# Performance work log

Hardware: AMD Instinct MI355X
Metric: run time of the kernel (lower is better)

Reference implementation:

```python
import jax, jax.numpy as jnp
import numpy as np

DIM = 768
EPS = 1e-06


def _layernorm(x, gamma, beta):
    # LayerNorm over last axis (channels), eps=EPS, elementwise affine
    mu = jnp.mean(x, axis=-1, keepdims=True)
    var = jnp.mean(jnp.square(x - mu), axis=-1, keepdims=True)
    return (x - mu) * jax.lax.rsqrt(var + EPS) * gamma + beta


def setup_inputs() -> dict:
    key = jax.random.key(0)
    ks = jax.random.split(key, 10)
    B, C, H, W = 16, DIM, 32, 32
    s = 1.0 / np.sqrt(C)  # mimic Conv2d default init scale
    return {
        "x": jax.random.normal(ks[0], (B, C, H, W), dtype=jnp.float32),
        "W1": jax.random.uniform(ks[1], (C, C), jnp.float32, -s, s),
        "b1": jax.random.uniform(ks[2], (C,), jnp.float32, -s, s),
        "g1": jnp.ones((C,), jnp.float32),
        "beta1": jnp.zeros((C,), jnp.float32),
        "W2": jax.random.uniform(ks[3], (C, C), jnp.float32, -s, s),
        "b2": jax.random.uniform(ks[4], (C,), jnp.float32, -s, s),
        "g2": jnp.ones((C,), jnp.float32),
        "beta2": jnp.zeros((C,), jnp.float32),
        "W3": jax.random.uniform(ks[5], (C, C), jnp.float32, -s, s),
        "b3": jax.random.uniform(ks[6], (C,), jnp.float32, -s, s),
    }


def reference(x, W1, b1, g1, beta1, W2, b2, g2, beta2, W3, b3):
    # x: [B, C, H, W] (NCHW). Work in NHWC; 1x1 conv == channel matmul.
    h = jnp.transpose(x, (0, 2, 3, 1))  # [B, H, W, C]
    h = jnp.einsum("bhwc,oc->bhwo", h, W1) + b1
    h = jax.nn.gelu(_layernorm(h, g1, beta1), approximate=False)
    h = jnp.einsum("bhwc,oc->bhwo", h, W2) + b2
    h = jax.nn.gelu(_layernorm(h, g2, beta2), approximate=False)
    h = jnp.einsum("bhwc,oc->bhwo", h, W3) + b3
    return jnp.transpose(h, (0, 3, 1, 2))  # back to NCHW
```

## Files before the change

### kernel.cpp

```cpp
#include <hip/hip_runtime.h>
#include <hip/hip_bf16.h>

typedef __bf16 bf16;
typedef __bf16 bf16x4 __attribute__((ext_vector_type(4)));
typedef __bf16 bf16x8 __attribute__((ext_vector_type(8)));
typedef float f32x4 __attribute__((ext_vector_type(4)));

#define DIM 768
#define HW 1024
#define BATCH 16
#define M_TOTAL (BATCH * HW)
#define NKT 24

#define AS1 __attribute__((address_space(1)))
#define AS3 __attribute__((address_space(3)))


__global__ void wcvt3_kernel(const float4* __restrict__ w1, const float4* __restrict__ w2,
                             const float4* __restrict__ w3,
                             bf16x8* __restrict__ o1, bf16x8* __restrict__ o2,
                             bf16x8* __restrict__ o3) {
    const int b = blockIdx.x;
    const int which = b / 288;
    const int i = (b % 288) * 256 + threadIdx.x;
    const float4* w = which == 0 ? w1 : which == 1 ? w2 : w3;
    bf16x8* o = which == 0 ? o1 : which == 1 ? o2 : o3;
    const int row = i / 96, br = i % 96;
    const int q = br >> 2, g = br & 3;
    float4 lo = w[row * 192 + q * 8 + g];
    float4 hi = w[row * 192 + q * 8 + g + 4];
    bf16x8 r = { (bf16)lo.x, (bf16)lo.y, (bf16)lo.z, (bf16)lo.w,
                 (bf16)hi.x, (bf16)hi.y, (bf16)hi.z, (bf16)hi.w };
    o[row * 96 + br] = r;
}

__global__ void transpose_cvt_kernel(const float* __restrict__ x, bf16* __restrict__ xb) {
    __shared__ float tile[32][33];
    const int b = blockIdx.z;
    const int hw0 = blockIdx.x * 32;
    const int c0 = blockIdx.y * 32;
    const int tx = threadIdx.x, ty = threadIdx.y;

    const float* src = x + ((size_t)b * DIM + c0) * HW + hw0;
#pragma unroll
    for (int j = 0; j < 4; j++)
        tile[ty + 8 * j][tx] = src[(size_t)(ty + 8 * j) * HW + tx];
    __syncthreads();
    const int ptx = (((tx & 15) >> 2) << 3) + (tx & 3) + ((tx >> 4) << 2);
    bf16* dst = xb + ((size_t)b * HW + hw0) * DIM + c0;
#pragma unroll
    for (int j = 0; j < 4; j++)
        dst[(size_t)(ty + 8 * j) * DIM + ptx] = (bf16)tile[tx][ty + 8 * j];
}

template <int MODE>
__global__ __launch_bounds__(256, 3) void gemm_kernel(
    const bf16* __restrict__ A,
    const bf16* __restrict__ Bw,
    const float* __restrict__ bias,
    void* __restrict__ out)
{
    constexpr int K = DIM;
    __shared__ bf16 As[3][128][32];
    __shared__ bf16 Bs[3][128][32];

    const int t = threadIdx.x;
    const int lane = t & 63;
    const int wave = t >> 6;
    const int wr = wave >> 1, wc = wave & 1;

    const int bid = blockIdx.x;
    const int virt = (bid & 7) * 96 + (bid >> 3);
    const int mI = virt / 6;
    const int m0 = mI * 128;
    const int n0 = (virt - mI * 6) * 128;

    const int fr = lane & 15;
    const int fq = lane >> 4;

    f32x4 acc[4][4] = {};

    const int sr = t >> 2;
    const int sb = t & 3;

    auto stage = [&](int kt, int buf) {
        const int k0 = kt * 32;
#pragma unroll
        for (int j = 0; j < 2; j++) {
            const int r = sr + j * 64;
            const int gs = sb ^ ((r ^ (r >> 2)) & 3);
            __builtin_amdgcn_global_load_lds(
                (const AS1 void*)(A + (size_t)(m0 + r) * K + k0 + gs * 8),
                (AS3 void*)&As[buf][r][sb * 8], 16, 0, 0);
            __builtin_amdgcn_global_load_lds(
                (const AS1 void*)(Bw + (size_t)(n0 + r) * K + k0 + gs * 8),
                (AS3 void*)&Bs[buf][r][sb * 8], 16, 0, 0);
        }
    };

    stage(0, 0);
    stage(1, 1);
    asm volatile("s_waitcnt vmcnt(4)" ::: "memory");
    __builtin_amdgcn_s_barrier();
    __builtin_amdgcn_sched_barrier(0);

    int c0 = 0, c1 = 1, c2 = 2;
    for (int kt = 0; kt < NKT; ++kt) {
        if (kt + 2 < NKT) stage(kt + 2, c2);

        bf16x8 aF[4], bF[4];
#pragma unroll
        for (int mi = 0; mi < 4; mi++) {
            const int R = wr * 64 + mi * 16 + fr;
            aF[mi] = *(const bf16x8*)(&As[c0][R][0] + ((fq ^ ((R ^ (R >> 2)) & 3)) << 3));
        }
#pragma unroll
        for (int ni = 0; ni < 4; ni++) {
            const int R = wc * 64 + ni * 16 + fr;
            bF[ni] = *(const bf16x8*)(&Bs[c0][R][0] + ((fq ^ ((R ^ (R >> 2)) & 3)) << 3));
        }
        __builtin_amdgcn_s_setprio(1);
#pragma unroll
        for (int mi = 0; mi < 4; mi++)
#pragma unroll
            for (int ni = 0; ni < 4; ni++)
                acc[mi][ni] = __builtin_amdgcn_mfma_f32_16x16x32_bf16(aF[mi], bF[ni], acc[mi][ni], 0, 0, 0);
        __builtin_amdgcn_s_setprio(0);

        if (kt < NKT - 1) {
            if (kt + 2 < NKT) { asm volatile("s_waitcnt vmcnt(4)" ::: "memory"); }
            else              { asm volatile("s_waitcnt vmcnt(0)" ::: "memory"); }
            __builtin_amdgcn_s_barrier();
            __builtin_amdgcn_sched_barrier(0);
        }
        const int tmp = c0; c0 = c1; c1 = c2; c2 = tmp;
    }

    if (MODE == 0) {
        bf16* o = (bf16*)out;
#pragma unroll
        for (int mi = 0; mi < 4; mi++) {
            const int row = m0 + wr * 64 + mi * 16 + fq * 4;
#pragma unroll
            for (int ni = 0; ni < 4; ni++) {
                const int col = n0 + wc * 64 + ni * 16 + fr;
                const int pcol = n0 + wc * 64 + ((ni >> 1) << 5) + ((fr >> 2) << 3)
                               + (fr & 3) + ((ni & 1) << 2);
                const float bv = bias[col];
#pragma unroll
                for (int r = 0; r < 4; r++)
                    o[(size_t)(row + r) * DIM + pcol] = (bf16)(acc[mi][ni][r] + bv);
            }
        }
    } else {
        float* o = (float*)out;
#pragma unroll
        for (int mi = 0; mi < 4; mi++) {
            const int nb = m0 + wr * 64 + mi * 16 + (lane >> 4) * 4;
            const int bI = nb >> 10, hw = nb & 1023;
#pragma unroll
            for (int ni = 0; ni < 4; ni++) {
                const int col = n0 + wc * 64 + ni * 16 + fr;
                f32x4 v = acc[mi][ni] + bias[col];
                *(f32x4*)(o + ((size_t)bI * DIM + col) * HW + hw) = v;
            }
        }
    }
}

__global__ __launch_bounds__(256) void ln_gelu_kernel(
    bf16* __restrict__ h, const float* __restrict__ g, const float* __restrict__ beta)
{
    const int wave = threadIdx.x >> 6;
    const int lane = threadIdx.x & 63;
    const int n = blockIdx.x * 4 + wave;
    bf16* row = h + (size_t)n * DIM;

    float v[12];
    float s = 0.f, ss = 0.f;
#pragma unroll
    for (int j = 0; j < 3; j++) {
        bf16x4 x = *(const bf16x4*)(row + j * 256 + lane * 4);
#pragma unroll
        for (int i = 0; i < 4; i++) {
            float f = (float)x[i];
            v[j * 4 + i] = f;
            s += f;
            ss += f * f;
        }
    }
#pragma unroll
    for (int off = 32; off > 0; off >>= 1) {
        s += __shfl_xor(s, off);
        ss += __shfl_xor(ss, off);
    }
    const float mu = s * (1.f / DIM);
    const float var = ss * (1.f / DIM) - mu * mu;
    const float rstd = rsqrtf(var + 1e-6f);

#pragma unroll
    for (int j = 0; j < 3; j++) {
        bf16x4 r;
#pragma unroll
        for (int i = 0; i < 4; i++) {
            const int c = j * 256 + lane * 4 + i;
            const int p = (lane * 4 + i) & 31;
            const int kk = ((p >> 3) << 2) + (p & 7) + ((p & 4) ? 12 : 0);
            const int gi = (c & ~31) + kk;
            float y = (v[j * 4 + i] - mu) * rstd * g[gi] + beta[gi];
            y = 0.5f * y * (1.f + erff(y * 0.70710678118f));
            r[i] = (bf16)y;
        }
        *(bf16x4*)(row + j * 256 + lane * 4) = r;
    }
}

extern "C" void kernel_launch(void* const* d_in, const int* in_sizes, int n_in,
                              void* d_out, int out_size, void* d_ws, size_t ws_size,
                              hipStream_t stream) {
    const float* x   = (const float*)d_in[0];
    const float* W1  = (const float*)d_in[1];
    const float* b1  = (const float*)d_in[2];
    const float* g1  = (const float*)d_in[3];
    const float* be1 = (const float*)d_in[4];
    const float* W2  = (const float*)d_in[5];
    const float* b2  = (const float*)d_in[6];
    const float* g2  = (const float*)d_in[7];
    const float* be2 = (const float*)d_in[8];
    const float* W3  = (const float*)d_in[9];
    const float* b3  = (const float*)d_in[10];
    float* out = (float*)d_out;

    bf16* Wb1  = (bf16*)d_ws;
    bf16* Wb2  = Wb1 + (size_t)DIM * DIM;
    bf16* Wb3  = Wb2 + (size_t)DIM * DIM;
    bf16* buf0 = Wb3 + (size_t)DIM * DIM;
    bf16* buf1 = buf0 + (size_t)M_TOTAL * DIM;

    wcvt3_kernel<<<864, 256, 0, stream>>>((const float4*)W1, (const float4*)W2, (const float4*)W3,
                                          (bf16x8*)Wb1, (bf16x8*)Wb2, (bf16x8*)Wb3);

    transpose_cvt_kernel<<<dim3(32, 24, 16), dim3(32, 8), 0, stream>>>(x, buf0);

    const int ggrid = (M_TOTAL / 128) * (DIM / 128);
    gemm_kernel<0><<<ggrid, 256, 0, stream>>>(buf0, Wb1, b1, buf1);
    ln_gelu_kernel<<<M_TOTAL / 4, 256, 0, stream>>>(buf1, g1, be1);
    gemm_kernel<0><<<ggrid, 256, 0, stream>>>(buf1, Wb2, b2, buf0);
    ln_gelu_kernel<<<M_TOTAL / 4, 256, 0, stream>>>(buf0, g2, be2);
    gemm_kernel<1><<<ggrid, 256, 0, stream>>>(buf0, Wb3, b3, out);
}
```

Baseline: 163.7 us.

## Retile GEMM to 64x192 double-buffered tiles and merge prep kernels

The GEMM tile changes from 128x128 with a triple-buffered pipeline to 64x192 with double buffering in one shared LDS array. Each of the four waves now covers all 64 rows and a 48-column slice, the grid grows to 1024 blocks, and launch bounds rise to allow four blocks per CU. The weight conversion and input transpose kernels are merged into one launch to save a kernel dispatch. The smaller tile lowers arithmetic intensity per LDS load, and the shallower pipeline waits vmcnt(0) every iteration, trading prefetch depth for occupancy.

```diff
diff --git a/kernel.cpp b/kernel.cpp
--- a/kernel.cpp
+++ b/kernel.cpp
@@ -16,136 +16,132 @@
 #define AS3 __attribute__((address_space(3)))
 
 
-__global__ void wcvt3_kernel(const float4* __restrict__ w1, const float4* __restrict__ w2,
-                             const float4* __restrict__ w3,
-                             bf16x8* __restrict__ o1, bf16x8* __restrict__ o2,
-                             bf16x8* __restrict__ o3) {
-    const int b = blockIdx.x;
-    const int which = b / 288;
-    const int i = (b % 288) * 256 + threadIdx.x;
-    const float4* w = which == 0 ? w1 : which == 1 ? w2 : w3;
-    bf16x8* o = which == 0 ? o1 : which == 1 ? o2 : o3;
-    const int row = i / 96, br = i % 96;
-    const int q = br >> 2, g = br & 3;
-    float4 lo = w[row * 192 + q * 8 + g];
-    float4 hi = w[row * 192 + q * 8 + g + 4];
-    bf16x8 r = { (bf16)lo.x, (bf16)lo.y, (bf16)lo.z, (bf16)lo.w,
-                 (bf16)hi.x, (bf16)hi.y, (bf16)hi.z, (bf16)hi.w };
-    o[row * 96 + br] = r;
-}
-
-__global__ void transpose_cvt_kernel(const float* __restrict__ x, bf16* __restrict__ xb) {
+__global__ void prep_kernel(const float* __restrict__ x, bf16* __restrict__ xb,
+                            const float4* __restrict__ w1, const float4* __restrict__ w2,
+                            const float4* __restrict__ w3,
+                            bf16x8* __restrict__ o1, bf16x8* __restrict__ o2,
+                            bf16x8* __restrict__ o3) {
     __shared__ float tile[32][33];
-    const int b = blockIdx.z;
-    const int hw0 = blockIdx.x * 32;
-    const int c0 = blockIdx.y * 32;
-    const int tx = threadIdx.x, ty = threadIdx.y;
-
-    const float* src = x + ((size_t)b * DIM + c0) * HW + hw0;
-#pragma unroll
-    for (int j = 0; j < 4; j++)
-        tile[ty + 8 * j][tx] = src[(size_t)(ty + 8 * j) * HW + tx];
-    __syncthreads();
-    const int ptx = (((tx & 15) >> 2) << 3) + (tx & 3) + ((tx >> 4) << 2);
-    bf16* dst = xb + ((size_t)b * HW + hw0) * DIM + c0;
-#pragma unroll
-    for (int j = 0; j < 4; j++)
-        dst[(size_t)(ty + 8 * j) * DIM + ptx] = (bf16)tile[tx][ty + 8 * j];
+    if (blockIdx.x < 864) {
+        const int b = blockIdx.x;
+        const int which = b / 288;
+        const int i = (b % 288) * 256 + threadIdx.x;
+        const float4* w = which == 0 ? w1 : which == 1 ? w2 : w3;
+        bf16x8* o = which == 0 ? o1 : which == 1 ? o2 : o3;
+        const int row = i / 96, br = i % 96;
+        const int q = br >> 2, g = br & 3;
+        float4 lo = w[row * 192 + q * 8 + g];
+        float4 hi = w[row * 192 + q * 8 + g + 4];
+        bf16x8 r = { (bf16)lo.x, (bf16)lo.y, (bf16)lo.z, (bf16)lo.w,
+                     (bf16)hi.x, (bf16)hi.y, (bf16)hi.z, (bf16)hi.w };
+        o[row * 96 + br] = r;
+    } else {
+        const int e = blockIdx.x - 864;
+        const int b = e / 768;
+        const int rem = e % 768;
+        const int c0 = (rem / 32) * 32;
+        const int hw0 = (rem % 32) * 32;
+        const int tx = threadIdx.x & 31, ty = threadIdx.x >> 5;
+
+        const float* src = x + ((size_t)b * DIM + c0) * HW + hw0;
+#pragma unroll
+        for (int j = 0; j < 4; j++)
+            tile[ty + 8 * j][tx] = src[(size_t)(ty + 8 * j) * HW + tx];
+        __syncthreads();
+        const int ptx = (((tx & 15) >> 2) << 3) + (tx & 3) + ((tx >> 4) << 2);
+        bf16* dst = xb + ((size_t)b * HW + hw0) * DIM + c0;
+#pragma unroll
+        for (int j = 0; j < 4; j++)
+            dst[(size_t)(ty + 8 * j) * DIM + ptx] = (bf16)tile[tx][ty + 8 * j];
+    }
 }
 
 template <int MODE>
-__global__ __launch_bounds__(256, 3) void gemm_kernel(
+__global__ __launch_bounds__(256, 4) void gemm_kernel(
     const bf16* __restrict__ A,
     const bf16* __restrict__ Bw,
     const float* __restrict__ bias,
     void* __restrict__ out)
 {
     constexpr int K = DIM;
-    __shared__ bf16 As[3][128][32];
-    __shared__ bf16 Bs[3][128][32];
+    __shared__ bf16 S[2][256][32];
 
     const int t = threadIdx.x;
     const int lane = t & 63;
-    const int wave = t >> 6;
-    const int wr = wave >> 1, wc = wave & 1;
+    const int w = t >> 6;
 
     const int bid = blockIdx.x;
-    const int virt = (bid & 7) * 96 + (bid >> 3);
-    const int mI = virt / 6;
-    const int m0 = mI * 128;
-    const int n0 = (virt - mI * 6) * 128;
-
-    const int fr = lane & 15;
-    const int fq = lane >> 4;
-
-    f32x4 acc[4][4] = {};
-
-    const int sr = t >> 2;
-    const int sb = t & 3;
+    const int virt = (bid & 7) * 128 + (bid >> 3);
+    const int m0 = (virt >> 2) * 64;
+    const int n0 = (virt & 3) * 192;
+
+    const int fr = lane & 15, fq = lane >> 4;
+
+    f32x4 acc[4][3] = {};
+
+    const int sg = t & 3;
 
     auto stage = [&](int kt, int buf) {
         const int k0 = kt * 32;
 #pragma unroll
-        for (int j = 0; j < 2; j++) {
-            const int r = sr + j * 64;
-            const int gs = sb ^ ((r ^ (r >> 2)) & 3);
-            __builtin_amdgcn_global_load_lds(
-                (const AS1 void*)(A + (size_t)(m0 + r) * K + k0 + gs * 8),
-                (AS3 void*)&As[buf][r][sb * 8], 16, 0, 0);
-            __builtin_amdgcn_global_load_lds(
-                (const AS1 void*)(Bw + (size_t)(n0 + r) * K + k0 + gs * 8),
-                (AS3 void*)&Bs[buf][r][sb * 8], 16, 0, 0);
+        for (int j = 0; j < 4; j++) {
+            const int r = j * 64 + (t >> 2);
+            const int gs = sg ^ ((r ^ (r >> 2)) & 3);
+            const bf16* src = (j == 0)
+                ? (A  + (size_t)(m0 + r) * K + k0 + gs * 8)
+                : (Bw + (size_t)(n0 + r - 64) * K + k0 + gs * 8);
+            __builtin_amdgcn_global_load_lds((const AS1 void*)src,
+                (AS3 void*)&S[buf][r][sg * 8], 16, 0, 0);
         }
     };
 
     stage(0, 0);
-    stage(1, 1);
-    asm volatile("s_waitcnt vmcnt(4)" ::: "memory");
+    asm volatile("s_waitcnt vmcnt(0)" ::: "memory");
     __builtin_amdgcn_s_barrier();
     __builtin_amdgcn_sched_barrier(0);
 
-    int c0 = 0, c1 = 1, c2 = 2;
+    int cur = 0;
     for (int kt = 0; kt < NKT; ++kt) {
-        if (kt + 2 < NKT) stage(kt + 2, c2);
-
-        bf16x8 aF[4], bF[4];
+        bf16x8 aF[4], bF[3];
 #pragma unroll
         for (int mi = 0; mi < 4; mi++) {
-            const int R = wr * 64 + mi * 16 + fr;
-            aF[mi] = *(const bf16x8*)(&As[c0][R][0] + ((fq ^ ((R ^ (R >> 2)) & 3)) << 3));
-        }
-#pragma unroll
-        for (int ni = 0; ni < 4; ni++) {
-            const int R = wc * 64 + ni * 16 + fr;
-            bF[ni] = *(const bf16x8*)(&Bs[c0][R][0] + ((fq ^ ((R ^ (R >> 2)) & 3)) << 3));
-        }
+            const int R = mi * 16 + fr;
+            aF[mi] = *(const bf16x8*)(&S[cur][R][0] + ((fq ^ ((R ^ (R >> 2)) & 3)) << 3));
+        }
+#pragma unroll
+        for (int ni = 0; ni < 3; ni++) {
+            const int R = 64 + w * 48 + ni * 16 + fr;
+            bF[ni] = *(const bf16x8*)(&S[cur][R][0] + ((fq ^ ((R ^ (R >> 2)) & 3)) << 3));
+        }
+        if (kt + 1 < NKT) stage(kt + 1, cur ^ 1);
+
         __builtin_amdgcn_s_setprio(1);
 #pragma unroll
         for (int mi = 0; mi < 4; mi++)
 #pragma unroll
-            for (int ni = 0; ni < 4; ni++)
+            for (int ni = 0; ni < 3; ni++)
                 acc[mi][ni] = __builtin_amdgcn_mfma_f32_16x16x32_bf16(aF[mi], bF[ni], acc[mi][ni], 0, 0, 0);
         __builtin_amdgcn_s_setprio(0);
 
-        if (kt < NKT - 1) {
-            if (kt + 2 < NKT) { asm volatile("s_waitcnt vmcnt(4)" ::: "memory"); }
-            else              { asm volatile("s_waitcnt vmcnt(0)" ::: "memory"); }
+        if (kt + 1 < NKT) {
+            asm volatile("s_waitcnt vmcnt(0)" ::: "memory");
             __builtin_amdgcn_s_barrier();
             __builtin_amdgcn_sched_barrier(0);
         }
-        const int tmp = c0; c0 = c1; c1 = c2; c2 = tmp;
+        cur ^= 1;
     }
 
     if (MODE == 0) {
         bf16* o = (bf16*)out;
 #pragma unroll
         for (int mi = 0; mi < 4; mi++) {
-            const int row = m0 + wr * 64 + mi * 16 + fq * 4;
-#pragma unroll
-            for (int ni = 0; ni < 4; ni++) {
-                const int col = n0 + wc * 64 + ni * 16 + fr;
-                const int pcol = n0 + wc * 64 + ((ni >> 1) << 5) + ((fr >> 2) << 3)
-                               + (fr & 3) + ((ni & 1) << 2);
+            const int row = m0 + mi * 16 + fq * 4;
+#pragma unroll
+            for (int ni = 0; ni < 3; ni++) {
+                const int off = w * 48 + ni * 16;
+                const int col = n0 + off + fr;
+                const int pcol = n0 + (off & ~31) + ((fr >> 2) << 3) + (fr & 3)
+                               + (((off >> 4) & 1) << 2);
                 const float bv = bias[col];
 #pragma unroll
                 for (int r = 0; r < 4; r++)
@@ -156,11 +152,11 @@
         float* o = (float*)out;
 #pragma unroll
         for (int mi = 0; mi < 4; mi++) {
-            const int nb = m0 + wr * 64 + mi * 16 + (lane >> 4) * 4;
+            const int nb = m0 + mi * 16 + fq * 4;
             const int bI = nb >> 10, hw = nb & 1023;
 #pragma unroll
-            for (int ni = 0; ni < 4; ni++) {
-                const int col = n0 + wc * 64 + ni * 16 + fr;
+            for (int ni = 0; ni < 3; ni++) {
+                const int col = n0 + w * 48 + ni * 16 + fr;
                 f32x4 v = acc[mi][ni] + bias[col];
                 *(f32x4*)(o + ((size_t)bI * DIM + col) * HW + hw) = v;
             }
@@ -237,12 +233,11 @@
     bf16* buf0 = Wb3 + (size_t)DIM * DIM;
     bf16* buf1 = buf0 + (size_t)M_TOTAL * DIM;
 
-    wcvt3_kernel<<<864, 256, 0, stream>>>((const float4*)W1, (const float4*)W2, (const float4*)W3,
-                                          (bf16x8*)Wb1, (bf16x8*)Wb2, (bf16x8*)Wb3);
-
-    transpose_cvt_kernel<<<dim3(32, 24, 16), dim3(32, 8), 0, stream>>>(x, buf0);
-
-    const int ggrid = (M_TOTAL / 128) * (DIM / 128);
+    prep_kernel<<<864 + 12288, 256, 0, stream>>>(
+        x, buf0, (const float4*)W1, (const float4*)W2, (const float4*)W3,
+        (bf16x8*)Wb1, (bf16x8*)Wb2, (bf16x8*)Wb3);
+
+    const int ggrid = (M_TOTAL / 64) * (DIM / 192);
     gemm_kernel<0><<<ggrid, 256, 0, stream>>>(buf0, Wb1, b1, buf1);
     ln_gelu_kernel<<<M_TOTAL / 4, 256, 0, stream>>>(buf1, g1, be1);
     gemm_kernel<0><<<ggrid, 256, 0, stream>>>(buf1, Wb2, b2, buf0);
```

New measurement: 169.8 us. 3.7% more time.
